# Performance work log

Hardware: AMD Instinct MI355X
Metric: run time of the kernel (lower is better)

## Reference

```python
import jax, jax.numpy as jnp
import numpy as np
import math

D_MODEL = 1024
N_HEADS = 16
D_HEAD = D_MODEL // N_HEADS
B, T = 2, 2048


def setup_inputs() -> dict:
    key = jax.random.key(0)
    ks = jax.random.split(key, 5)
    x = jax.random.normal(ks[0], (B, T, D_MODEL), dtype=jnp.float32)
    W_qkv = jax.random.normal(ks[1], (D_MODEL, 3 * D_MODEL), dtype=jnp.float32) * 0.02
    b_qkv = jnp.zeros((3 * D_MODEL,), dtype=jnp.float32)
    W_g = jax.random.normal(ks[2], (N_HEADS, D_HEAD, D_HEAD), dtype=jnp.float32) * 0.02
    W_out = jax.random.normal(ks[3], (D_MODEL, D_MODEL), dtype=jnp.float32) * 0.02
    b_out = jnp.zeros((D_MODEL,), dtype=jnp.float32)
    return {"x": x, "W_qkv": W_qkv, "b_qkv": b_qkv, "W_g": W_g, "W_out": W_out, "b_out": b_out}


def reference(x, W_qkv, b_qkv, W_g, W_out, b_out):
    b, t, d = x.shape
    h, dh = N_HEADS, D_HEAD
    qkv = x @ W_qkv + b_qkv                         # (B,T,3D)
    q, k, v = jnp.split(qkv, 3, axis=-1)
    # (B,T,D) -> (B,H,T,dh)
    q = q.reshape(b, t, h, dh).transpose(0, 2, 1, 3)
    k = k.reshape(b, t, h, dh).transpose(0, 2, 1, 3)
    v = v.reshape(b, t, h, dh).transpose(0, 2, 1, 3)
    scale = 1.0 / math.sqrt(dh)
    scores = jnp.einsum('bhtd,bhsd->bhts', q, k) * scale   # (B,H,T,T)
    causal = jnp.tril(jnp.ones((t, t), dtype=bool))
    scores = jnp.where(causal, scores, jnp.float32(-jnp.inf))
    attn = jax.nn.softmax(scores, axis=-1)
    # query-conditioned bilinear value gate (applied at each position)
    g = jax.nn.sigmoid(jnp.einsum('bhtd,hde->bhte', q, W_g))  # (B,H,T,dh)
    v = g * v
    out = jnp.einsum('bhts,bhsd->bhtd', attn, v)             # (B,H,T,dh)
    out = out.transpose(0, 2, 1, 3).reshape(b, t, d)
    return out @ W_out + b_out
```

## Files before the change

### kernel.cpp

```cpp
#include <hip/hip_runtime.h>
#include <hip/hip_bf16.h>

typedef unsigned short ushortT;
typedef __bf16 bf16x8 __attribute__((ext_vector_type(8)));
typedef __bf16 bf16x4 __attribute__((ext_vector_type(4)));
typedef float f32x4 __attribute__((ext_vector_type(4)));

#define T_SEQ 2048
#define DH 64
#define NH 16
#define DM 1024
#define TD 3072
#define BATCH 2
#define LOG2E 1.44269504f

#define BARRIER()   asm volatile("s_barrier" ::: "memory")
#define VMCNT(n)    asm volatile("s_waitcnt vmcnt(" #n ")" ::: "memory")

__device__ inline ushortT f2bf(float f){
    union { float f; unsigned int u; } a; a.f = f;
    unsigned int r = a.u + 0x7fffu + ((a.u >> 16) & 1u);
    return (ushortT)(r >> 16);
}
__device__ inline float bf2f(ushortT u){
    union { float f; unsigned int u; } a; a.u = ((unsigned int)u) << 16;
    return a.f;
}

__device__ inline void gload_lds16(const void* g, void* l){
    __builtin_amdgcn_global_load_lds((const __attribute__((address_space(1))) void*)g,
                                     (__attribute__((address_space(3))) void*)l, 16, 0, 0);
}

__global__ __launch_bounds__(256) void cast_bf16_kernel(const float* __restrict__ in,
                                                        ushortT* __restrict__ out, int n){
    int i = (blockIdx.x * 256 + threadIdx.x) * 4;
    if (i < n){
        float4 v = *(const float4*)&in[i];
        out[i+0] = f2bf(v.x); out[i+1] = f2bf(v.y);
        out[i+2] = f2bf(v.z); out[i+3] = f2bf(v.w);
    }
}

__global__ __launch_bounds__(256) void transcast_kernel(const float* __restrict__ in,
                                                        ushortT* __restrict__ out, int K, int N){
    __shared__ float tile[64][65];
    int n0 = blockIdx.x * 64, k0 = blockIdx.y * 64;
    int tid = threadIdx.x;
    int c  = tid & 63;
    int r4 = tid >> 6;
#pragma unroll
    for (int i = 0; i < 16; i++){
        int k = r4 + i * 4;
        tile[k][c] = in[(size_t)(k0 + k) * N + n0 + c];
    }
    __syncthreads();
#pragma unroll
    for (int i = 0; i < 16; i++){
        int n = r4 + i * 4;
        out[(size_t)(n0 + n) * K + k0 + c] = f2bf(tile[c][n]);
    }
}

__global__ __launch_bounds__(256) void wg_transcast_kernel(const float* __restrict__ in,
                                                           ushortT* __restrict__ out){
    __shared__ float tile[64][65];
    int h = blockIdx.x;
    int tid = threadIdx.x;
    int c = tid & 63, r4 = tid >> 6;
#pragma unroll
    for (int i = 0; i < 16; i++){
        int d = r4 + i*4;
        tile[d][c] = in[h*4096 + d*64 + c];
    }
    __syncthreads();
#pragma unroll
    for (int i = 0; i < 16; i++){
        int e = r4 + i*4;
        out[h*4096 + e*64 + c] = f2bf(tile[c][e]);
    }
}

__device__ inline void store_out(ushortT* C, size_t i, float v){ C[i] = f2bf(v); }
__device__ inline void store_out(float*   C, size_t i, float v){ C[i] = v; }

template <typename OUT>
__global__ __launch_bounds__(256) void gemm_bf16_kernel(const ushortT* __restrict__ A,
                                                        const ushortT* __restrict__ BT,
                                                        const float* __restrict__ bias,
                                                        OUT* __restrict__ C,
                                                        int M, int N, int K){
    __shared__ __align__(16) ushortT As[2][128*32];
    __shared__ __align__(16) ushortT Bs[2][128*32];
    int tid = threadIdx.x;
    int m0 = blockIdx.x * 128;
    int n0 = blockIdx.y * 128;
    int wid = tid >> 6, lane = tid & 63;
    int l15 = lane & 15, g = lane >> 4;
    int wr = wid >> 1, wc = wid & 1;

    f32x4 acc[4][4];
#pragma unroll
    for (int i = 0; i < 4; i++)
#pragma unroll
        for (int j = 0; j < 4; j++) acc[i][j] = (f32x4){0.f,0.f,0.f,0.f};

    int srow = wid * 32 + (lane >> 2);
    int sch  = lane & 3;

#define GSTAGE(buf, k0)                                                                  \
    {                                                                                    \
        _Pragma("unroll")                                                                \
        for (int i_ = 0; i_ < 2; i_++){                                                  \
            int row_ = srow + i_ * 16;                                                   \
            const ushortT* asrc_ = A  + (size_t)(m0 + row_) * K + (k0) + sch * 8;        \
            const ushortT* bsrc_ = BT + (size_t)(n0 + row_) * K + (k0) + sch * 8;        \
            gload_lds16(asrc_, (char*)As[buf] + (wid*2 + i_) * 1024);                    \
            gload_lds16(bsrc_, (char*)Bs[buf] + (wid*2 + i_) * 1024);                    \
        }                                                                                \
    }

    GSTAGE(0, 0);

    int nk = K >> 5;
    for (int kt = 0; kt < nk; kt++){
        int buf = kt & 1;
        BARRIER();
        if (kt + 1 < nk){
            GSTAGE(buf ^ 1, (kt + 1) * 32);
            VMCNT(4);
        } else {
            VMCNT(0);
        }
        BARRIER();

        bf16x8 af[4], bfr[4];
#pragma unroll
        for (int mi = 0; mi < 4; mi++){
            int r = wr*64 + mi*16 + l15;
            af[mi]  = *(const bf16x8*)(As[buf] + r*32 + g*8);
        }
#pragma unroll
        for (int ni = 0; ni < 4; ni++){
            int r = wc*64 + ni*16 + l15;
            bfr[ni] = *(const bf16x8*)(Bs[buf] + r*32 + g*8);
        }
#pragma unroll
        for (int mi = 0; mi < 4; mi++)
#pragma unroll
            for (int ni = 0; ni < 4; ni++)
                acc[mi][ni] = __builtin_amdgcn_mfma_f32_16x16x32_bf16(af[mi], bfr[ni], acc[mi][ni], 0, 0, 0);
    }
#undef GSTAGE

#pragma unroll
    for (int mi = 0; mi < 4; mi++){
#pragma unroll
        for (int jj = 0; jj < 4; jj++){
            int mm = m0 + wr*64 + mi*16 + 4*g + jj;
#pragma unroll
            for (int ni = 0; ni < 4; ni++){
                int nn = n0 + wc*64 + ni*16 + l15;
                float v = acc[mi][ni][jj] + bias[nn];
                store_out(C, (size_t)mm * N + nn, v);
            }
        }
    }
}

__global__ __launch_bounds__(256) void gate_kernel(const ushortT* __restrict__ qkv,
                                                   const ushortT* __restrict__ WgT,
                                                   ushortT* __restrict__ vgT){
    __shared__ __align__(16) ushortT VT[64][72];
    int tblk = blockIdx.x, bh = blockIdx.y;
    int b = bh >> 4, h = bh & 15;
    int tid = threadIdx.x, wid = tid >> 6, lane = tid & 63;
    int l15 = lane & 15, g = lane >> 4;
    int t0 = tblk * 64;
    int tl = wid*16 + l15;

    const ushortT* qrow = qkv + ((size_t)b*T_SEQ + t0 + tl)*TD + h*DH;
    bf16x8 qf0 = *(const bf16x8*)(qrow + 8*g);
    bf16x8 qf1 = *(const bf16x8*)(qrow + 32 + 8*g);

    const ushortT* wbase = WgT + h*4096;
    const ushortT* vrow = qkv + ((size_t)b*T_SEQ + t0 + tl)*TD + 2*DM + h*DH;

#pragma unroll
    for (int ns = 0; ns < 4; ns++){
        int e = ns*16 + l15;
        bf16x8 wf0 = *(const bf16x8*)(wbase + e*64 + 8*g);
        bf16x8 wf1 = *(const bf16x8*)(wbase + e*64 + 32 + 8*g);
        f32x4 z = (f32x4){0.f,0.f,0.f,0.f};
        z = __builtin_amdgcn_mfma_f32_16x16x32_bf16(wf0, qf0, z, 0, 0, 0);
        z = __builtin_amdgcn_mfma_f32_16x16x32_bf16(wf1, qf1, z, 0, 0, 0);
        union { ushortT u[4]; uint2 v; } v4;
        v4.v = *(const uint2*)(vrow + ns*16 + 4*g);
#pragma unroll
        for (int jj = 0; jj < 4; jj++){
            float ex = __builtin_amdgcn_exp2f(-z[jj] * LOG2E);
            float gv = __builtin_amdgcn_rcpf(1.f + ex);
            VT[ns*16 + 4*g + jj][tl] = f2bf(gv * bf2f(v4.u[jj]));
        }
    }
    __syncthreads();
    for (int i = tid; i < 64*8; i += 256){
        int e = i >> 3, c8 = (i & 7) * 8;
        *(uint4*)&vgT[((size_t)bh * DH + e) * T_SEQ + t0 + c8] = *(const uint4*)&VT[e][c8];
    }
}

struct QS {
    bf16x8 qf0, qf1;
    float m_, lsum;
    f32x4 acc[4];
};

__device__ __forceinline__ void softmax_state(f32x4* s, QS& S, bool diag,
                                              int wq, int l15, int g,
                                              bf16x8& pa0, bf16x8& pa1){
    float tmax = -INFINITY;
    if (diag){
        int qrel = wq*16 + l15;
#pragma unroll
        for (int ns = 0; ns < 4; ns++){
            int kbase = ((ns & 2) << 4) + 8*g + ((ns & 1) << 2);
#pragma unroll
            for (int jj = 0; jj < 4; jj++){
                if (kbase + jj > qrel) s[ns][jj] = -INFINITY;
                tmax = fmaxf(tmax, s[ns][jj]);
            }
        }
    } else {
#pragma unroll
        for (int ns = 0; ns < 4; ns++){
            float a = fmaxf(s[ns][0], s[ns][1]);
            float c = fmaxf(s[ns][2], s[ns][3]);
            tmax = fmaxf(tmax, fmaxf(a, c));
        }
    }
    tmax = fmaxf(tmax, __shfl_xor(tmax, 16, 64));
    tmax = fmaxf(tmax, __shfl_xor(tmax, 32, 64));

    float mnew = fmaxf(S.m_, tmax);
    float mc = mnew * LOG2E;
    float rs = 0.f;
#pragma unroll
    for (int jj = 0; jj < 4; jj++){
        float p0 = __builtin_amdgcn_exp2f(fmaf(s[0][jj], LOG2E, -mc));
        float p1 = __builtin_amdgcn_exp2f(fmaf(s[1][jj], LOG2E, -mc));
        float p2 = __builtin_amdgcn_exp2f(fmaf(s[2][jj], LOG2E, -mc));
        float p3 = __builtin_amdgcn_exp2f(fmaf(s[3][jj], LOG2E, -mc));
        rs += (p0 + p1) + (p2 + p3);
        pa0[jj]   = (__bf16)p0;
        pa0[4+jj] = (__bf16)p1;
        pa1[jj]   = (__bf16)p2;
        pa1[4+jj] = (__bf16)p3;
    }
    rs += __shfl_xor(rs, 16, 64);
    rs += __shfl_xor(rs, 32, 64);

    if (!__all(mnew == S.m_)){
        float alpha = __builtin_amdgcn_exp2f(fmaf(S.m_, LOG2E, -mc));
#pragma unroll
        for (int nt = 0; nt < 4; nt++)
#pragma unroll
            for (int jj = 0; jj < 4; jj++) S.acc[nt][jj] *= alpha;
        S.lsum *= alpha;
        S.m_ = mnew;
    }
    S.lsum += rs;
}

__device__ __forceinline__ void proc_tile1(const ushortT* __restrict__ Kb,
                                           const ushortT* __restrict__ Vb,
                                           QS& S, bool diag,
                                           int wq, int l15, int g){
    int l7 = l15 & 7;
    f32x4 s[4];
    __builtin_amdgcn_s_setprio(1);
#pragma unroll
    for (int ns = 0; ns < 4; ns++){
        int kr = ns*16 + l15;
        bf16x8 kf0 = *(const bf16x8*)(Kb + kr*64 + ((g    ) ^ l7)*8);
        bf16x8 kf1 = *(const bf16x8*)(Kb + kr*64 + ((4 + g) ^ l7)*8);
        f32x4 z = (f32x4){0.f,0.f,0.f,0.f};
        z = __builtin_amdgcn_mfma_f32_16x16x32_bf16(kf0, S.qf0, z, 0, 0, 0);
        z = __builtin_amdgcn_mfma_f32_16x16x32_bf16(kf1, S.qf1, z, 0, 0, 0);
        s[ns] = z;
    }
    __builtin_amdgcn_s_setprio(0);

    bf16x8 pa0, pa1;
    softmax_state(s, S, diag, wq, l15, g, pa0, pa1);

    __builtin_amdgcn_s_setprio(1);
#pragma unroll
    for (int ks = 0; ks < 2; ks++){
        bf16x8 pa = ks ? pa1 : pa0;
#pragma unroll
        for (int nt = 0; nt < 4; nt++){
            bf16x8 vf = *(const bf16x8*)(Vb + (nt*16 + l15)*64 + ((ks*4 + g) ^ l7)*8);
            S.acc[nt] = __builtin_amdgcn_mfma_f32_16x16x32_bf16(vf, pa, S.acc[nt], 0, 0, 0);
        }
    }
    __builtin_amdgcn_s_setprio(0);
}

__global__ __launch_bounds__(512, 4) void attn_kernel(const ushortT* __restrict__ qkv,
                                                      const ushortT* __restrict__ vgT,
                                                      ushortT* __restrict__ obf){
    __shared__ __align__(16) ushortT Ks[2][2][64*64];
    __shared__ __align__(16) ushortT Vs[2][2][64*64];
    int id = blockIdx.x;
    int bh = id & 31;
    int y  = id >> 5;
    int ya = y & 7, yb = y >> 3;
    int qblk = yb*8 + ((yb & 1) ? 7 - ya : ya);
    int b = bh >> 4, h = bh & 15;
    int tid = threadIdx.x, wid = tid >> 6, lane = tid & 63;
    int l15 = lane & 15, g = lane >> 4;
    int grp = wid >> 2;
    int wq  = wid & 3;

    const ushortT* Kg = qkv + (size_t)b * T_SEQ * TD + DM + h * DH;
    const ushortT* Vg = vgT + (size_t)bh * DH * T_SEQ;

    int st_row  = tid >> 3;
    int st_c    = (tid & 7) ^ (st_row & 7);
    int st_prow = (st_row & 0x20) | ((st_row & 0x0C) << 1) |
                  ((st_row & 0x10) >> 2) | (st_row & 3);

#define STAGE_PAIR(buf, rr)                                                              \
    {                                                                                    \
        int keT_ = 2*(rr);     if (keT_ > qblk) keT_ = qblk;                             \
        int koT_ = 2*(rr) + 1; if (koT_ > qblk) koT_ = qblk;                             \
        int kvE_ = keT_ * 64, kvO_ = koT_ * 64;                                          \
        gload_lds16(Kg + (size_t)(kvE_ + st_prow) * TD + st_c*8,                         \
                    (char*)Ks[buf][0] + wid*1024);                                       \
        gload_lds16(Kg + (size_t)(kvO_ + st_prow) * TD + st_c*8,                         \
                    (char*)Ks[buf][1] + wid*1024);                                       \
        gload_lds16(Vg + (size_t)st_row * T_SEQ + kvE_ + st_c*8,                         \
                    (char*)Vs[buf][0] + wid*1024);                                       \
        gload_lds16(Vg + (size_t)st_row * T_SEQ + kvO_ + st_c*8,                         \
                    (char*)Vs[buf][1] + wid*1024);                                       \
    }

    QS S;
    {
        int qrow = qblk*64 + wq*16 + l15;
        const ushortT* qb = qkv + ((size_t)b * T_SEQ + qrow) * TD + h * DH;
        S.qf0 = *(const bf16x8*)(qb + 8*g);
        S.qf1 = *(const bf16x8*)(qb + 32 + 8*g);
#pragma unroll
        for (int j = 0; j < 8; j++){
            S.qf0[j] = (__bf16)((float)S.qf0[j] * 0.125f);
            S.qf1[j] = (__bf16)((float)S.qf1[j] * 0.125f);
        }
        S.m_ = -INFINITY; S.lsum = 0.f;
#pragma unroll
        for (int nt = 0; nt < 4; nt++) S.acc[nt] = (f32x4){0.f,0.f,0.f,0.f};
    }

    int nr = (qblk >> 1) + 1;
    STAGE_PAIR(0, 0);

    for (int r = 0; r < nr; r++){
        int buf = r & 1;
        BARRIER();
        if (r + 1 < nr){
            STAGE_PAIR(buf ^ 1, r + 1);
            VMCNT(4);
        } else {
            VMCNT(0);
        }
        BARRIER();
        int t = 2*r + grp;
        if (t <= qblk)
            proc_tile1(Ks[buf][grp], Vs[buf][grp], S, t == qblk, wq, l15, g);
    }
#undef STAGE_PAIR

    BARRIER();
    float* accL = (float*)&Ks[0][0][0];
    float* mlL  = (float*)&Vs[0][0][0];
    if (grp == 1){
        mlL[(wq*2 + 0)*16 + l15] = S.m_;
        mlL[(wq*2 + 1)*16 + l15] = S.lsum;
#pragma unroll
        for (int nt = 0; nt < 4; nt++)
#pragma unroll
            for (int jj = 0; jj < 4; jj++)
                accL[wq*1024 + (nt*16 + 4*g + jj)*16 + l15] = S.acc[nt][jj];
    }
    BARRIER();
    if (grp == 0){
        float m2 = mlL[(wq*2 + 0)*16 + l15];
        float l2 = mlL[(wq*2 + 1)*16 + l15];
        float mm = fmaxf(S.m_, m2);
        float a1 = __builtin_amdgcn_exp2f((S.m_ - mm) * LOG2E);
        float a2 = __builtin_amdgcn_exp2f((m2  - mm) * LOG2E);
        float inv = 1.f / (S.lsum * a1 + l2 * a2);
        float ia1 = a1 * inv, ia2 = a2 * inv;
        size_t orow = ((size_t)b * T_SEQ + qblk*64 + wq*16 + l15) * DM + h*DH;
#pragma unroll
        for (int nt = 0; nt < 4; nt++){
            union { ushortT u[4]; uint2 v; } pk;
#pragma unroll
            for (int jj = 0; jj < 4; jj++){
                float o2 = accL[wq*1024 + (nt*16 + 4*g + jj)*16 + l15];
                pk.u[jj] = f2bf(S.acc[nt][jj] * ia1 + o2 * ia2);
            }
            *(uint2*)&obf[orow + nt*16 + 4*g] = pk.v;
        }
    }
}

extern "C" void kernel_launch(void* const* d_in, const int* in_sizes, int n_in,
                              void* d_out, int out_size, void* d_ws, size_t ws_size,
                              hipStream_t stream){
    const float* x    = (const float*)d_in[0];
    const float* Wqkv = (const float*)d_in[1];
    const float* bqkv = (const float*)d_in[2];
    const float* Wg   = (const float*)d_in[3];
    const float* Wout = (const float*)d_in[4];
    const float* bout = (const float*)d_in[5];

    char* ws = (char*)d_ws;
    ushortT* xbf   = (ushortT*)(ws);
    ushortT* wqkvT = (ushortT*)(ws + 8388608);
    ushortT* woutT = (ushortT*)(ws + 14680064);
    ushortT* qkvb  = (ushortT*)(ws + 16777216);
    ushortT* vgT   = (ushortT*)(ws + 41943040);
    ushortT* obf   = (ushortT*)(ws + 50331648);
    ushortT* wgT   = (ushortT*)(ws + 58720256);

    cast_bf16_kernel<<<4096, 256, 0, stream>>>(x, xbf, 4194304);
    transcast_kernel<<<dim3(48,16), 256, 0, stream>>>(Wqkv, wqkvT, 1024, 3072);
    transcast_kernel<<<dim3(16,16), 256, 0, stream>>>(Wout, woutT, 1024, 1024);
    wg_transcast_kernel<<<16, 256, 0, stream>>>(Wg, wgT);
    gemm_bf16_kernel<ushortT><<<dim3(32,24), 256, 0, stream>>>(xbf, wqkvT, bqkv, qkvb, 4096, 3072, 1024);
    gate_kernel<<<dim3(32,32), 256, 0, stream>>>(qkvb, wgT, vgT);
    attn_kernel<<<1024, 512, 0, stream>>>(qkvb, vgT, obf);
    gemm_bf16_kernel<float><<<dim3(32,8), 256, 0, stream>>>(obf, woutT, bout, (float*)d_out, 4096, 1024, 1024);
}
```

Before: 124.7 us.

## Use 256x256-tile pipelined GEMM with swizzled LDS for QKV projection

Adds a new 512-thread GEMM kernel with 256x256 output tiles and K-step 64 for the QKV projection. It uses direct global-to-LDS loads with XOR-swizzled chunks, double buffering with staged prefetch interleaved across four compute phases, and s_setprio around the MFMA bursts. The larger tile is meant to raise arithmetic intensity and overlap loads with compute. In exchange the grid shrinks to 192 blocks, which leaves some of the 256 CUs idle, and each block needs 128KB of LDS.

After: 130.0 us. 1.04x slower.

```diff
diff --git a/kernel.cpp b/kernel.cpp
--- a/kernel.cpp
+++ b/kernel.cpp
@@ -81,8 +81,115 @@
     }
 }
 
-__device__ inline void store_out(ushortT* C, size_t i, float v){ C[i] = f2bf(v); }
-__device__ inline void store_out(float*   C, size_t i, float v){ C[i] = v; }
+__global__ __launch_bounds__(512) void gemm256_kernel(const ushortT* __restrict__ A,
+                                                      const ushortT* __restrict__ BT,
+                                                      const float* __restrict__ bias,
+                                                      ushortT* __restrict__ C,
+                                                      int M, int N, int K){
+    __shared__ __align__(16) ushortT As[2][256*64];
+    __shared__ __align__(16) ushortT Bs[2][256*64];
+    int tid = threadIdx.x;
+    int m0 = blockIdx.x * 256;
+    int n0 = blockIdx.y * 256;
+    int wid = tid >> 6, lane = tid & 63;
+    int l15 = lane & 15, g = lane >> 4;
+    int l7 = l15 & 7;
+    int wm = wid >> 2, wn = wid & 3;
+
+    f32x4 acc[8][4];
+#pragma unroll
+    for (int i = 0; i < 8; i++)
+#pragma unroll
+        for (int j = 0; j < 4; j++) acc[i][j] = (f32x4){0.f,0.f,0.f,0.f};
+
+    int rb = tid >> 3;
+    int lch = (tid & 7) ^ (rb & 7);
+
+#define STAGE_A(buf, k0_, i_)                                                            \
+    gload_lds16(A  + (size_t)(m0 + (i_)*64 + rb) * K + (k0_) + lch*8,                    \
+                (char*)As[buf] + ((i_)*512 + tid) * 16)
+#define STAGE_B(buf, k0_, i_)                                                            \
+    gload_lds16(BT + (size_t)(n0 + (i_)*64 + rb) * K + (k0_) + lch*8,                    \
+                (char*)Bs[buf] + ((i_)*512 + tid) * 16)
+
+    STAGE_A(0, 0, 0); STAGE_A(0, 0, 1); STAGE_A(0, 0, 2); STAGE_A(0, 0, 3);
+    STAGE_B(0, 0, 0); STAGE_B(0, 0, 1); STAGE_B(0, 0, 2); STAGE_B(0, 0, 3);
+
+    int NK = K >> 6;
+    for (int kt = 0; kt < NK; kt++){
+        int b  = kt & 1;
+        int nb = b ^ 1;
+        int nk0 = (kt + 1) << 6;
+        bool more = (kt + 1 < NK);
+
+        if (more){
+            STAGE_A(nb, nk0, 0); STAGE_A(nb, nk0, 1);
+            VMCNT(2);
+        } else {
+            VMCNT(0);
+        }
+        BARRIER();
+
+        const ushortT* Ab = As[b];
+        const ushortT* Bb = Bs[b];
+        bf16x8 bf[4], af[4];
+
+#pragma unroll
+        for (int ph = 0; ph < 4; ph++){
+            int ks = ph >> 1;
+            int mh = ph & 1;
+            int cchunk = (ks*4 + g) ^ l7;
+            if (mh == 0){
+#pragma unroll
+                for (int ni = 0; ni < 4; ni++){
+                    int r = wn*64 + ni*16 + l15;
+                    bf[ni] = *(const bf16x8*)(Bb + r*64 + cchunk*8);
+                }
+            }
+#pragma unroll
+            for (int mi2 = 0; mi2 < 4; mi2++){
+                int r = wm*128 + (mh*4 + mi2)*16 + l15;
+                af[mi2] = *(const bf16x8*)(Ab + r*64 + cchunk*8);
+            }
+            if (more){
+                if (ph == 0){ STAGE_A(nb, nk0, 2); STAGE_A(nb, nk0, 3); }
+                else if (ph == 1){ STAGE_B(nb, nk0, 0); STAGE_B(nb, nk0, 1); }
+                else if (ph == 2){ STAGE_B(nb, nk0, 2); STAGE_B(nb, nk0, 3); }
+            }
+            BARRIER();
+            __builtin_amdgcn_s_setprio(1);
+#pragma unroll
+            for (int mi2 = 0; mi2 < 4; mi2++)
+#pragma unroll
+                for (int ni = 0; ni < 4; ni++)
+                    acc[mh*4 + mi2][ni] =
+                        __builtin_amdgcn_mfma_f32_16x16x32_bf16(af[mi2], bf[ni],
+                                                                acc[mh*4 + mi2][ni], 0, 0, 0);
+            __builtin_amdgcn_s_setprio(0);
+            BARRIER();
+        }
+    }
+#undef STAGE_A
+#undef STAGE_B
+
+#pragma unroll
+    for (int mi = 0; mi < 8; mi++){
+#pragma unroll
+        for (int jj = 0; jj < 4; jj++){
+            int mm = m0 + wm*128 + mi*16 + 4*g + jj;
+#pragma unroll
+            for (int ni = 0; ni < 4; ni++){
+                int nn = n0 + wn*64 + ni*16 + l15;
+                C[(size_t)mm * N + nn] = f2bf(acc[mi][ni][jj] + bias[nn]);
+            }
+        }
+    }
+}
+
+template <typename OUT>
+__device__ inline void store_out(OUT* C, size_t i, float v);
+template <> __device__ inline void store_out<ushortT>(ushortT* C, size_t i, float v){ C[i] = f2bf(v); }
+template <> __device__ inline void store_out<float>(float* C, size_t i, float v){ C[i] = v; }
 
 template <typename OUT>
 __global__ __launch_bounds__(256) void gemm_bf16_kernel(const ushortT* __restrict__ A,
@@ -162,7 +269,7 @@
             for (int ni = 0; ni < 4; ni++){
                 int nn = n0 + wc*64 + ni*16 + l15;
                 float v = acc[mi][ni][jj] + bias[nn];
-                store_out(C, (size_t)mm * N + nn, v);
+                store_out<OUT>(C, (size_t)mm * N + nn, v);
             }
         }
     }
@@ -439,7 +546,7 @@
     transcast_kernel<<<dim3(48,16), 256, 0, stream>>>(Wqkv, wqkvT, 1024, 3072);
     transcast_kernel<<<dim3(16,16), 256, 0, stream>>>(Wout, woutT, 1024, 1024);
     wg_transcast_kernel<<<16, 256, 0, stream>>>(Wg, wgT);
-    gemm_bf16_kernel<ushortT><<<dim3(32,24), 256, 0, stream>>>(xbf, wqkvT, bqkv, qkvb, 4096, 3072, 1024);
+    gemm256_kernel<<<dim3(16,12), 512, 0, stream>>>(xbf, wqkvT, bqkv, qkvb, 4096, 3072, 1024);
     gate_kernel<<<dim3(32,32), 256, 0, stream>>>(qkvb, wgT, vgT);
     attn_kernel<<<1024, 512, 0, stream>>>(qkvb, vgT, obf);
     gemm_bf16_kernel<float><<<dim3(32,8), 256, 0, stream>>>(obf, woutT, bout, (float*)d_out, 4096, 1024, 1024);
```

## Pair complementary query blocks per workgroup, each wave group processing two KV tiles

Applied to the files above, without the earlier changes.

The attention kernel now gives each workgroup two query blocks (p and 31-p) that share staged K/V tiles. Each wave group handles its own query block and processes both staged tiles per round. This replaces the old split where two wave groups shared one query block and merged partial softmax states through LDS at the end. The goal is balanced causal work per workgroup, half as many workgroups, and no cross-group reduction. The cost is extra register pressure (eight score tiles live, launch bounds lowered to 2) and idle work for the short query block in later rounds.

After: 118.9 us. -4.7%, faster.

```diff
diff --git a/kernel.cpp b/kernel.cpp
--- a/kernel.cpp
+++ b/kernel.cpp
@@ -216,107 +216,133 @@
     f32x4 acc[4];
 };
 
-__device__ __forceinline__ void softmax_state(f32x4* s, QS& S, bool diag,
-                                              int wq, int l15, int g,
-                                              bf16x8& pa0, bf16x8& pa1){
-    float tmax = -INFINITY;
-    if (diag){
-        int qrel = wq*16 + l15;
-#pragma unroll
-        for (int ns = 0; ns < 4; ns++){
-            int kbase = ((ns & 2) << 4) + 8*g + ((ns & 1) << 2);
-#pragma unroll
-            for (int jj = 0; jj < 4; jj++){
-                if (kbase + jj > qrel) s[ns][jj] = -INFINITY;
-                tmax = fmaxf(tmax, s[ns][jj]);
-            }
-        }
-    } else {
-#pragma unroll
-        for (int ns = 0; ns < 4; ns++){
-            float a = fmaxf(s[ns][0], s[ns][1]);
-            float c = fmaxf(s[ns][2], s[ns][3]);
-            tmax = fmaxf(tmax, fmaxf(a, c));
-        }
-    }
-    tmax = fmaxf(tmax, __shfl_xor(tmax, 16, 64));
-    tmax = fmaxf(tmax, __shfl_xor(tmax, 32, 64));
-
-    float mnew = fmaxf(S.m_, tmax);
-    float mc = mnew * LOG2E;
-    float rs = 0.f;
-#pragma unroll
-    for (int jj = 0; jj < 4; jj++){
-        float p0 = __builtin_amdgcn_exp2f(fmaf(s[0][jj], LOG2E, -mc));
-        float p1 = __builtin_amdgcn_exp2f(fmaf(s[1][jj], LOG2E, -mc));
-        float p2 = __builtin_amdgcn_exp2f(fmaf(s[2][jj], LOG2E, -mc));
-        float p3 = __builtin_amdgcn_exp2f(fmaf(s[3][jj], LOG2E, -mc));
-        rs += (p0 + p1) + (p2 + p3);
-        pa0[jj]   = (__bf16)p0;
-        pa0[4+jj] = (__bf16)p1;
-        pa1[jj]   = (__bf16)p2;
-        pa1[4+jj] = (__bf16)p3;
-    }
-    rs += __shfl_xor(rs, 16, 64);
-    rs += __shfl_xor(rs, 32, 64);
-
-    if (!__all(mnew == S.m_)){
-        float alpha = __builtin_amdgcn_exp2f(fmaf(S.m_, LOG2E, -mc));
-#pragma unroll
-        for (int nt = 0; nt < 4; nt++)
-#pragma unroll
-            for (int jj = 0; jj < 4; jj++) S.acc[nt][jj] *= alpha;
-        S.lsum *= alpha;
-        S.m_ = mnew;
-    }
-    S.lsum += rs;
-}
-
-__device__ __forceinline__ void proc_tile1(const ushortT* __restrict__ Kb,
-                                           const ushortT* __restrict__ Vb,
-                                           QS& S, bool diag,
-                                           int wq, int l15, int g){
+__device__ __forceinline__ void proc2(const ushortT* __restrict__ K0,
+                                      const ushortT* __restrict__ V0,
+                                      const ushortT* __restrict__ K1,
+                                      const ushortT* __restrict__ V1,
+                                      QS& S, int t0, int t1, int myp,
+                                      int wq, int l15, int g){
     int l7 = l15 & 7;
-    f32x4 s[4];
+    f32x4 s[8];
     __builtin_amdgcn_s_setprio(1);
 #pragma unroll
     for (int ns = 0; ns < 4; ns++){
         int kr = ns*16 + l15;
-        bf16x8 kf0 = *(const bf16x8*)(Kb + kr*64 + ((g    ) ^ l7)*8);
-        bf16x8 kf1 = *(const bf16x8*)(Kb + kr*64 + ((4 + g) ^ l7)*8);
+        bf16x8 kf0 = *(const bf16x8*)(K0 + kr*64 + ((g    ) ^ l7)*8);
+        bf16x8 kf1 = *(const bf16x8*)(K0 + kr*64 + ((4 + g) ^ l7)*8);
         f32x4 z = (f32x4){0.f,0.f,0.f,0.f};
         z = __builtin_amdgcn_mfma_f32_16x16x32_bf16(kf0, S.qf0, z, 0, 0, 0);
         z = __builtin_amdgcn_mfma_f32_16x16x32_bf16(kf1, S.qf1, z, 0, 0, 0);
         s[ns] = z;
     }
+#pragma unroll
+    for (int ns = 0; ns < 4; ns++){
+        int kr = ns*16 + l15;
+        bf16x8 kf0 = *(const bf16x8*)(K1 + kr*64 + ((g    ) ^ l7)*8);
+        bf16x8 kf1 = *(const bf16x8*)(K1 + kr*64 + ((4 + g) ^ l7)*8);
+        f32x4 z = (f32x4){0.f,0.f,0.f,0.f};
+        z = __builtin_amdgcn_mfma_f32_16x16x32_bf16(kf0, S.qf0, z, 0, 0, 0);
+        z = __builtin_amdgcn_mfma_f32_16x16x32_bf16(kf1, S.qf1, z, 0, 0, 0);
+        s[4 + ns] = z;
+    }
     __builtin_amdgcn_s_setprio(0);
 
-    bf16x8 pa0, pa1;
-    softmax_state(s, S, diag, wq, l15, g, pa0, pa1);
+    int qrel = wq*16 + l15;
+    bool diag0 = (t0 == myp);
+    bool inv1  = (t1 > myp);
+    bool diag1 = (t1 == myp);
+    if (diag0){
+#pragma unroll
+        for (int ns = 0; ns < 4; ns++){
+            int kb = ((ns & 2) << 4) + 8*g + ((ns & 1) << 2);
+#pragma unroll
+            for (int jj = 0; jj < 4; jj++)
+                if (kb + jj > qrel) s[ns][jj] = -INFINITY;
+        }
+    }
+    if (inv1){
+#pragma unroll
+        for (int ns = 0; ns < 4; ns++)
+#pragma unroll
+            for (int jj = 0; jj < 4; jj++) s[4+ns][jj] = -INFINITY;
+    } else if (diag1){
+#pragma unroll
+        for (int ns = 0; ns < 4; ns++){
+            int kb = ((ns & 2) << 4) + 8*g + ((ns & 1) << 2);
+#pragma unroll
+            for (int jj = 0; jj < 4; jj++)
+                if (kb + jj > qrel) s[4+ns][jj] = -INFINITY;
+        }
+    }
+
+    float tmax = -INFINITY;
+#pragma unroll
+    for (int ns = 0; ns < 8; ns++){
+        float a = fmaxf(s[ns][0], s[ns][1]);
+        float c = fmaxf(s[ns][2], s[ns][3]);
+        tmax = fmaxf(tmax, fmaxf(a, c));
+    }
+    tmax = fmaxf(tmax, __shfl_xor(tmax, 16, 64));
+    tmax = fmaxf(tmax, __shfl_xor(tmax, 32, 64));
+
+    float mnew = fmaxf(S.m_, tmax);
+    float mc = mnew * LOG2E;
+    float rs = 0.f;
+    bf16x8 pa[4];
+#pragma unroll
+    for (int pr = 0; pr < 4; pr++){
+#pragma unroll
+        for (int jj = 0; jj < 4; jj++){
+            float p0 = __builtin_amdgcn_exp2f(fmaf(s[2*pr  ][jj], LOG2E, -mc));
+            float p1 = __builtin_amdgcn_exp2f(fmaf(s[2*pr+1][jj], LOG2E, -mc));
+            rs += p0 + p1;
+            pa[pr][jj]   = (__bf16)p0;
+            pa[pr][4+jj] = (__bf16)p1;
+        }
+    }
+    rs += __shfl_xor(rs, 16, 64);
+    rs += __shfl_xor(rs, 32, 64);
+
+    if (!__all(mnew == S.m_)){
+        float alpha = __builtin_amdgcn_exp2f(fmaf(S.m_, LOG2E, -mc));
+#pragma unroll
+        for (int nt = 0; nt < 4; nt++)
+#pragma unroll
+            for (int jj = 0; jj < 4; jj++) S.acc[nt][jj] *= alpha;
+        S.lsum *= alpha;
+        S.m_ = mnew;
+    }
+    S.lsum += rs;
 
     __builtin_amdgcn_s_setprio(1);
 #pragma unroll
     for (int ks = 0; ks < 2; ks++){
-        bf16x8 pa = ks ? pa1 : pa0;
 #pragma unroll
         for (int nt = 0; nt < 4; nt++){
-            bf16x8 vf = *(const bf16x8*)(Vb + (nt*16 + l15)*64 + ((ks*4 + g) ^ l7)*8);
-            S.acc[nt] = __builtin_amdgcn_mfma_f32_16x16x32_bf16(vf, pa, S.acc[nt], 0, 0, 0);
+            bf16x8 vf = *(const bf16x8*)(V0 + (nt*16 + l15)*64 + ((ks*4 + g) ^ l7)*8);
+            S.acc[nt] = __builtin_amdgcn_mfma_f32_16x16x32_bf16(vf, pa[ks], S.acc[nt], 0, 0, 0);
+        }
+    }
+    if (!inv1){
+#pragma unroll
+        for (int ks = 0; ks < 2; ks++){
+#pragma unroll
+            for (int nt = 0; nt < 4; nt++){
+                bf16x8 vf = *(const bf16x8*)(V1 + (nt*16 + l15)*64 + ((ks*4 + g) ^ l7)*8);
+                S.acc[nt] = __builtin_amdgcn_mfma_f32_16x16x32_bf16(vf, pa[2+ks], S.acc[nt], 0, 0, 0);
+            }
         }
     }
     __builtin_amdgcn_s_setprio(0);
 }
 
-__global__ __launch_bounds__(512, 4) void attn_kernel(const ushortT* __restrict__ qkv,
+__global__ __launch_bounds__(512, 2) void attn_kernel(const ushortT* __restrict__ qkv,
                                                       const ushortT* __restrict__ vgT,
                                                       ushortT* __restrict__ obf){
     __shared__ __align__(16) ushortT Ks[2][2][64*64];
     __shared__ __align__(16) ushortT Vs[2][2][64*64];
-    int id = blockIdx.x;
-    int bh = id & 31;
-    int y  = id >> 5;
-    int ya = y & 7, yb = y >> 3;
-    int qblk = yb*8 + ((yb & 1) ? 7 - ya : ya);
+    int bh = blockIdx.x, y = blockIdx.y;
+    int pairid = (y < 8) ? y : 23 - y;
     int b = bh >> 4, h = bh & 15;
     int tid = threadIdx.x, wid = tid >> 6, lane = tid & 63;
     int l15 = lane & 15, g = lane >> 4;
@@ -326,29 +352,31 @@
     const ushortT* Kg = qkv + (size_t)b * T_SEQ * TD + DM + h * DH;
     const ushortT* Vg = vgT + (size_t)bh * DH * T_SEQ;
 
+    int pA = pairid, pB = 31 - pairid;
+    int myp = grp ? pB : pA;
+
     int st_row  = tid >> 3;
     int st_c    = (tid & 7) ^ (st_row & 7);
     int st_prow = (st_row & 0x20) | ((st_row & 0x0C) << 1) |
                   ((st_row & 0x10) >> 2) | (st_row & 3);
 
-#define STAGE_PAIR(buf, rr)                                                              \
+#define STAGE_ROUND(buf, rr)                                                             \
     {                                                                                    \
-        int keT_ = 2*(rr);     if (keT_ > qblk) keT_ = qblk;                             \
-        int koT_ = 2*(rr) + 1; if (koT_ > qblk) koT_ = qblk;                             \
-        int kvE_ = keT_ * 64, kvO_ = koT_ * 64;                                          \
-        gload_lds16(Kg + (size_t)(kvE_ + st_prow) * TD + st_c*8,                         \
-                    (char*)Ks[buf][0] + wid*1024);                                       \
-        gload_lds16(Kg + (size_t)(kvO_ + st_prow) * TD + st_c*8,                         \
-                    (char*)Ks[buf][1] + wid*1024);                                       \
-        gload_lds16(Vg + (size_t)st_row * T_SEQ + kvE_ + st_c*8,                         \
-                    (char*)Vs[buf][0] + wid*1024);                                       \
-        gload_lds16(Vg + (size_t)st_row * T_SEQ + kvO_ + st_c*8,                         \
-                    (char*)Vs[buf][1] + wid*1024);                                       \
+        int t0_ = 2*(rr);     if (t0_ > pB) t0_ = pB;                                    \
+        int t1_ = 2*(rr) + 1; if (t1_ > pB) t1_ = pB;                                    \
+        gload_lds16(Kg + (size_t)(t0_*64 + st_prow) * TD + st_c*8,                       \
+                    (char*)Ks[buf][0] + tid*16);                                         \
+        gload_lds16(Kg + (size_t)(t1_*64 + st_prow) * TD + st_c*8,                       \
+                    (char*)Ks[buf][1] + tid*16);                                         \
+        gload_lds16(Vg + (size_t)st_row * T_SEQ + t0_*64 + st_c*8,                       \
+                    (char*)Vs[buf][0] + tid*16);                                         \
+        gload_lds16(Vg + (size_t)st_row * T_SEQ + t1_*64 + st_c*8,                       \
+                    (char*)Vs[buf][1] + tid*16);                                         \
     }
 
     QS S;
     {
-        int qrow = qblk*64 + wq*16 + l15;
+        int qrow = myp*64 + wq*16 + l15;
         const ushortT* qb = qkv + ((size_t)b * T_SEQ + qrow) * TD + h * DH;
         S.qf0 = *(const bf16x8*)(qb + 8*g);
         S.qf1 = *(const bf16x8*)(qb + 32 + 8*g);
@@ -362,57 +390,34 @@
         for (int nt = 0; nt < 4; nt++) S.acc[nt] = (f32x4){0.f,0.f,0.f,0.f};
     }
 
-    int nr = (qblk >> 1) + 1;
-    STAGE_PAIR(0, 0);
+    int nr = (33 - pairid) >> 1;
+    STAGE_ROUND(0, 0);
 
     for (int r = 0; r < nr; r++){
         int buf = r & 1;
         BARRIER();
         if (r + 1 < nr){
-            STAGE_PAIR(buf ^ 1, r + 1);
+            STAGE_ROUND(buf ^ 1, r + 1);
             VMCNT(4);
         } else {
             VMCNT(0);
         }
         BARRIER();
-        int t = 2*r + grp;
-        if (t <= qblk)
-            proc_tile1(Ks[buf][grp], Vs[buf][grp], S, t == qblk, wq, l15, g);
-    }
-#undef STAGE_PAIR
-
-    BARRIER();
-    float* accL = (float*)&Ks[0][0][0];
-    float* mlL  = (float*)&Vs[0][0][0];
-    if (grp == 1){
-        mlL[(wq*2 + 0)*16 + l15] = S.m_;
-        mlL[(wq*2 + 1)*16 + l15] = S.lsum;
-#pragma unroll
-        for (int nt = 0; nt < 4; nt++)
-#pragma unroll
-            for (int jj = 0; jj < 4; jj++)
-                accL[wq*1024 + (nt*16 + 4*g + jj)*16 + l15] = S.acc[nt][jj];
-    }
-    BARRIER();
-    if (grp == 0){
-        float m2 = mlL[(wq*2 + 0)*16 + l15];
-        float l2 = mlL[(wq*2 + 1)*16 + l15];
-        float mm = fmaxf(S.m_, m2);
-        float a1 = __builtin_amdgcn_exp2f((S.m_ - mm) * LOG2E);
-        float a2 = __builtin_amdgcn_exp2f((m2  - mm) * LOG2E);
-        float inv = 1.f / (S.lsum * a1 + l2 * a2);
-        float ia1 = a1 * inv, ia2 = a2 * inv;
-        size_t orow = ((size_t)b * T_SEQ + qblk*64 + wq*16 + l15) * DM + h*DH;
-#pragma unroll
-        for (int nt = 0; nt < 4; nt++){
-            union { ushortT u[4]; uint2 v; } pk;
-#pragma unroll
-            for (int jj = 0; jj < 4; jj++){
-                float o2 = accL[wq*1024 + (nt*16 + 4*g + jj)*16 + l15];
-                pk.u[jj] = f2bf(S.acc[nt][jj] * ia1 + o2 * ia2);
-            }
-            *(uint2*)&obf[orow + nt*16 + 4*g] = pk.v;
-        }
+        int t0 = 2*r;
+        if (t0 <= myp)
+            proc2(Ks[buf][0], Vs[buf][0], Ks[buf][1], Vs[buf][1],
+                  S, t0, t0 + 1, myp, wq, l15, g);
+    }
+#undef STAGE_ROUND
+
+    float inv = 1.f / S.lsum;
+    size_t orow = ((size_t)b * T_SEQ + myp*64 + wq*16 + l15) * DM + h*DH;
+#pragma unroll
+    for (int nt = 0; nt < 4; nt++){
+        union { ushortT u[4]; uint2 v; } pk;
+#pragma unroll
+        for (int jj = 0; jj < 4; jj++) pk.u[jj] = f2bf(S.acc[nt][jj] * inv);
+        *(uint2*)&obf[orow + nt*16 + 4*g] = pk.v;
     }
 }
 
@@ -441,6 +446,6 @@
     wg_transcast_kernel<<<16, 256, 0, stream>>>(Wg, wgT);
     gemm_bf16_kernel<ushortT><<<dim3(32,24), 256, 0, stream>>>(xbf, wqkvT, bqkv, qkvb, 4096, 3072, 1024);
     gate_kernel<<<dim3(32,32), 256, 0, stream>>>(qkvb, wgT, vgT);
-    attn_kernel<<<1024, 512, 0, stream>>>(qkvb, vgT, obf);
+    attn_kernel<<<dim3(32,16), 512, 0, stream>>>(qkvb, vgT, obf);
     gemm_bf16_kernel<float><<<dim3(32,8), 256, 0, stream>>>(obf, woutT, bout, (float*)d_out, 4096, 1024, 1024);
 }
```
